# Performance work log

Measured on AMD Instinct MI355X. Metric: run time of the kernel, lower is better.

## Reference

```python
import jax, jax.numpy as jnp
import numpy as np

N_ROOMS = 300
N = N_ROOMS + 2          # state dim: 2 envelope nodes + rooms
M = N_ROOMS + 1          # input dim: [Tout; Q per room]
T = 60000                # number of t_eval points
DT = 30.0                # seconds between solution points
N_KNOTS = 2001           # Tout interpolation knots
ONE_THIRD = 1.0 / 3.0


def setup_inputs() -> dict:
    key = jax.random.key(0)
    k1, k2, k3, k4 = jax.random.split(key, 4)
    n_params = N * N + N_ROOMS
    params = jax.random.uniform(k1, (n_params,), jnp.float32)
    theta_lo = jnp.zeros((n_params,), jnp.float32)
    # conductance-like entries kept tiny so RK4 with h=30s stays stable
    theta_hi = jnp.concatenate([
        jnp.full((N * N,), 1e-4, jnp.float32),
        jnp.ones((N_ROOMS,), jnp.float32),
    ])
    B = jax.random.normal(k2, (N, M), jnp.float32) * 1e-3  # constant input matrix
    tout_t = jnp.linspace(0.0, T * DT, N_KNOTS).astype(jnp.float32)
    tout_vals = 15.0 + 10.0 * jax.random.normal(k3, (N_KNOTS,), jnp.float32)
    iv = 15.0 + 10.0 * jax.random.uniform(k4, (N, 1), jnp.float32)
    t_eval = jnp.arange(T, dtype=jnp.float32) * DT
    return {"params": params, "theta_lo": theta_lo, "theta_hi": theta_hi,
            "B": B, "tout_t": tout_t, "tout_vals": tout_vals,
            "iv": iv, "t_eval": t_eval, "t0": 0}


def reference(params, theta_lo, theta_hi, B, tout_t, tout_vals, iv, t_eval, t0):
    # transform + physical scaling of raw parameters
    x = jax.nn.sigmoid(params)
    theta = theta_lo + (theta_hi - theta_lo) * x
    W = theta[: N * N].reshape(N, N)
    # RC conductance matrix: diagonally dominant, negative diagonal (stable)
    A = W - jnp.diag(jnp.abs(W).sum(axis=1))
    Q = theta[N * N:]  # per-room heat gains [N_ROOMS]

    def f(t, y):
        # dy/dt = A y + B u,  u = [Tout(t + t0); Q]
        Tout = jnp.interp(t + t0, tout_t, tout_vals)
        u = jnp.concatenate([Tout[None], Q])[:, None]  # [M, 1]
        return A @ y + B @ u

    def step(y, th):
        # torchdiffeq method='rk4' uses the 3/8-rule (rk4_alt_step_func)
        t, h = th
        k1 = f(t, y)
        k2 = f(t + h * ONE_THIRD, y + h * ONE_THIRD * k1)
        k3 = f(t + 2.0 * h * ONE_THIRD, y + h * (k2 - ONE_THIRD * k1))
        k4 = f(t + h, y + h * (k1 - k2 + k3))
        y1 = y + (k1 + 3.0 * (k2 + k3) + k4) * (h * 0.125)
        return y1, y1

    ts = t_eval[:-1]
    hs = t_eval[1:] - t_eval[:-1]
    _, ys = jax.lax.scan(step, iv, (ts, hs))
    return jnp.concatenate([iv[None], ys], axis=0)  # [T, N, 1]
```

## Files before the change

kernel.cpp:

```cpp
#include <hip/hip_runtime.h>
#include <math.h>

#define NN     302
#define MM     301
#define NROOMS 300
#define NP     320
#define TS     59999
#define KN     2001
#define DTH    30.0f

#define L_CHUNK 256
#define N_CHUNK 235
#define N_BND   234
#define NB_PAD  240
#define N_GRP   15

#define WS_M    0
#define WS_M2   102400
#define WS_P    307200
#define WS_UV   409600
#define WS_B0C  411200
#define WS_TAU  412160
#define WS_W    652160
#define WS_G    1061760
#define WS_Y    1138560
#define WS_Z    1213760
#define WS_SA   1218880
#define WS_SB   1257280
#define WS_PL   1276480
#define WS_PA   1378880
#define WS_PB   1481280
#define WS_PT   1583680
#define WS_MT   2914880

typedef float vf2 __attribute__((ext_vector_type(2)));

#define ENGINE_BOUNDS __launch_bounds__(512) __attribute__((amdgpu_waves_per_eu(2, 2)))
#define PKFMA(acc, a, b) asm("v_pk_fma_f32 %0, %1, %2, %0" : "+v"(acc) : "v"(a), "v"(b))
#define PIN4(a, b, c, d) asm volatile("" : "+v"(a), "+v"(b), "+v"(c), "+v"(d))

__global__ __launch_bounds__(320) void buildrow_kernel(
    const float* __restrict__ params, const float* __restrict__ tlo,
    const float* __restrict__ thi, float* __restrict__ M, float* __restrict__ MT)
{
    const int r = blockIdx.x;
    const int c = threadIdx.x;
    float wv = 0.0f;
    if (r < NN && c < NN) {
        const int idx = r * NN + c;
        const float x = 1.0f / (1.0f + expf(-params[idx]));
        wv = tlo[idx] + (thi[idx] - tlo[idx]) * x;
    }
    __shared__ float red[5];
    float s = fabsf(wv);
    #pragma unroll
    for (int off = 32; off > 0; off >>= 1) s += __shfl_xor(s, off, 64);
    if ((c & 63) == 0) red[c >> 6] = s;
    __syncthreads();
    const float rs = red[0] + red[1] + red[2] + red[3] + red[4];
    float v = DTH * wv;
    if (r == c) v -= DTH * rs;
    M[r * NP + c] = v;
    MT[(size_t)c * NP + r] = v;
}

__global__ void b0c_kernel(const float* __restrict__ params,
                           const float* __restrict__ tlo,
                           const float* __restrict__ thi,
                           const float* __restrict__ B, float* __restrict__ b0c)
{
    __shared__ float Qs[NROOMS];
    const int r = blockIdx.x;
    const int l = threadIdx.x;
    for (int q = l; q < NROOMS; q += 64) {
        const int idx = NN * NN + q;
        const float x = 1.0f / (1.0f + expf(-params[idx]));
        Qs[q] = tlo[idx] + (thi[idx] - tlo[idx]) * x;
    }
    __syncthreads();
    if (r >= NN) {
        if (l == 0) { b0c[r] = 0.0f; b0c[NP + r] = 0.0f; }
        return;
    }
    float s = 0.0f;
    for (int q = l; q < NROOMS; q += 64) s = fmaf(B[r * MM + 1 + q], Qs[q], s);
    #pragma unroll
    for (int off = 32; off > 0; off >>= 1) s += __shfl_xor(s, off, 64);
    if (l == 0) { b0c[r] = B[r * MM]; b0c[NP + r] = s; }
}

__global__ void matmul4r(const float* __restrict__ A, const float* __restrict__ B,
                         float* __restrict__ C)
{
    const int c = blockIdx.x * 64 + threadIdx.x;
    const int r0 = blockIdx.y * 4;
    const float* Ar = A + (size_t)r0 * NP;
    float a0 = 0.f, a1 = 0.f, a2 = 0.f, a3 = 0.f;
    #pragma unroll 4
    for (int k = 0; k < NP; ++k) {
        const float b = B[(size_t)k * NP + c];
        a0 = fmaf(Ar[k], b, a0);
        a1 = fmaf(Ar[NP + k], b, a1);
        a2 = fmaf(Ar[2 * NP + k], b, a2);
        a3 = fmaf(Ar[3 * NP + k], b, a3);
    }
    C[(size_t)r0 * NP + c] = a0;
    C[(size_t)(r0 + 1) * NP + c] = a1;
    C[(size_t)(r0 + 2) * NP + c] = a2;
    C[(size_t)(r0 + 3) * NP + c] = a3;
}

__global__ void matmulP(const float* __restrict__ M2, const float* __restrict__ M,
                        float* __restrict__ P, float* __restrict__ PT0)
{
    const int c = blockIdx.x * 64 + threadIdx.x;
    const int r0 = blockIdx.y * 4;
    const float* Ar = M2 + (size_t)r0 * NP;
    float a0 = 0.f, a1 = 0.f, a2 = 0.f, a3 = 0.f;
    #pragma unroll 4
    for (int k = 0; k < NP; ++k) {
        const size_t o = (size_t)k * NP + c;
        const float b = (1.0f / 6.0f) * M[o] + (1.0f / 24.0f) * M2[o];
        a0 = fmaf(Ar[k], b, a0);
        a1 = fmaf(Ar[NP + k], b, a1);
        a2 = fmaf(Ar[2 * NP + k], b, a2);
        a3 = fmaf(Ar[3 * NP + k], b, a3);
    }
    float acc[4] = {a0, a1, a2, a3};
    float4 t;
    #pragma unroll
    for (int u = 0; u < 4; ++u) {
        const int r = r0 + u;
        const size_t idx = (size_t)r * NP + c;
        float v = acc[u] + M[idx] + 0.5f * M2[idx];
        if (r == c && r < NN) v += 1.0f;
        P[idx] = v;
        ((float*)&t)[u] = v;
    }
    *(float4*)(PT0 + (size_t)c * NP + r0) = t;
}

__global__ __launch_bounds__(320) void vec_kernel(
    const float* __restrict__ MT, const float* __restrict__ b0c,
    float* __restrict__ uv, const float* __restrict__ iv,
    float* __restrict__ W, float* __restrict__ out)
{
    __shared__ float ysB[NP], ysC[NP];
    const int tid = threadIdx.x;
    const float s = DTH / 8.0f;

    const float b0 = b0c[tid];
    const float cc = b0c[NP + tid];
    ysB[tid] = b0; ysC[tid] = cc;
    __syncthreads();

    float mb, mc, m2b, m2c, m3b, m3c;
    {
        float aB = 0.f, aC = 0.f;
        for (int k = 0; k < NP; ++k) {
            const float a = MT[(size_t)k * NP + tid];
            aB = fmaf(a, ysB[k], aB);
            aC = fmaf(a, ysC[k], aC);
        }
        mb = aB; mc = aC;
    }
    __syncthreads(); ysB[tid] = mb; ysC[tid] = mc; __syncthreads();
    {
        float aB = 0.f, aC = 0.f;
        for (int k = 0; k < NP; ++k) {
            const float a = MT[(size_t)k * NP + tid];
            aB = fmaf(a, ysB[k], aB);
            aC = fmaf(a, ysC[k], aC);
        }
        m2b = aB; m2c = aC;
    }
    __syncthreads(); ysB[tid] = m2b; ysC[tid] = m2c; __syncthreads();
    {
        float aB = 0.f, aC = 0.f;
        for (int k = 0; k < NP; ++k) {
            const float a = MT[(size_t)k * NP + tid];
            aB = fmaf(a, ysB[k], aB);
            aC = fmaf(a, ysC[k], aC);
        }
        m3b = aB; m3c = aC;
    }

    const float u1 = s * (b0 + mb + (1.0f / 3.0f) * (m2b + m3b));
    const float u2 = s * (3.0f * b0 + 2.0f * mb + m2b);
    const float u3 = s * (3.0f * b0 + mb);
    const float u4 = s * b0;
    const float dd = s * (8.0f * cc + 4.0f * mc + (4.0f / 3.0f) * m2c + (1.0f / 3.0f) * m3c);

    uv[tid]          = u1;
    uv[NP + tid]     = u2;
    uv[2 * NP + tid] = u3;
    uv[3 * NP + tid] = u4;
    uv[4 * NP + tid] = dd;

    W[(size_t)(0 << 8) * NP + tid] = dd;
    W[(size_t)(1 << 8) * NP + tid] = u1;
    W[(size_t)(2 << 8) * NP + tid] = u2;
    W[(size_t)(3 << 8) * NP + tid] = u3;
    W[(size_t)(4 << 8) * NP + tid] = u4;

    if (tid < NN) out[tid] = iv[tid];
}

__global__ void tau_kernel(const float* __restrict__ tout_t,
                           const float* __restrict__ tout_v,
                           const int* __restrict__ t0p,
                           float4* __restrict__ tau)
{
    const int n = blockIdx.x * 256 + threadIdx.x;
    if (n >= TS) return;
    const float tbase = 30.0f * (float)n + (float)(*t0p);
    float r[4];
    #pragma unroll
    for (int st = 0; st < 4; ++st) {
        const float x = tbase + 10.0f * (float)st;
        float res;
        if (x <= tout_t[0])            res = tout_v[0];
        else if (x >= tout_t[KN - 1])  res = tout_v[KN - 1];
        else {
            int k = (int)(x * (1.0f / 900.0f));
            if (k > KN - 2) k = KN - 2;
            if (k < 0) k = 0;
            if (x < tout_t[k] && k > 0) --k;
            else if (x >= tout_t[k + 1] && k < KN - 2) ++k;
            const float tk = tout_t[k], tk1 = tout_t[k + 1];
            const float wgt = (x - tk) / (tk1 - tk);
            res = tout_v[k] + wgt * (tout_v[k + 1] - tout_v[k]);
        }
        r[st] = res;
    }
    tau[n] = make_float4(r[0], r[1], r[2], r[3]);
}

__global__ __launch_bounds__(320) void fat_kernel(
    const float* __restrict__ src, float* __restrict__ dst,
    float* __restrict__ PTall, int j, float* __restrict__ W,
    const float* __restrict__ Sin, float* __restrict__ Sout, int npairs)
{
    const int b = blockIdx.x;
    const int tid = threadIdx.x;
    if (b < 320) {
        const int w = tid >> 6, l = tid & 63;
        const int r = (b & 63) * 5 + w;
        const int c = (b >> 6) * 64 + l;
        const float* Ar = src + (size_t)r * NP;
        float acc = 0.f;
        #pragma unroll 4
        for (int k = 0; k < NP; ++k)
            acc = fmaf(Ar[k], src[(size_t)k * NP + c], acc);
        dst[(size_t)r * NP + c] = acc;
        PTall[(size_t)(j + 1) * NP * NP + (size_t)c * NP + r] = acc;
        return;
    }
    const float* PTj = PTall + (size_t)j * NP * NP;
    const int c0 = (b - 320) * 4;
    __shared__ float ys[4][NP];
    if (j < 8) {
        const int nc = 5 << j;
        #pragma unroll
        for (int u = 0; u < 4; ++u) {
            const int ci = c0 + u;
            float val = 0.0f;
            if (ci < nc) {
                const int v = ci >> j, mo = ci & ((1 << j) - 1);
                val = W[(size_t)((v << 8) + mo) * NP + tid];
            }
            ys[u][tid] = val;
        }
        __syncthreads();
        float a0 = 0.f, a1 = 0.f, a2 = 0.f, a3 = 0.f;
        #pragma unroll 4
        for (int k = 0; k < NP; ++k) {
            const float p = PTj[(size_t)k * NP + tid];
            a0 = fmaf(p, ys[0][k], a0);
            a1 = fmaf(p, ys[1][k], a1);
            a2 = fmaf(p, ys[2][k], a2);
            a3 = fmaf(p, ys[3][k], a3);
        }
        const float acc[4] = {a0, a1, a2, a3};
        #pragma unroll
        for (int u = 0; u < 4; ++u) {
            const int ci = c0 + u;
            if (ci < nc) {
                const int v = ci >> j, mo = ci & ((1 << j) - 1);
                W[(size_t)((v << 8) + (1 << j) + mo) * NP + tid] = acc[u];
            }
        }
    } else {
        #pragma unroll
        for (int u = 0; u < 4; ++u) {
            const int k = c0 + u;
            ys[u][tid] = (k < npairs) ? Sin[(size_t)(2 * k) * NP + tid] : 0.0f;
        }
        __syncthreads();
        float a0 = 0.f, a1 = 0.f, a2 = 0.f, a3 = 0.f;
        #pragma unroll 4
        for (int k = 0; k < NP; ++k) {
            const float p = PTj[(size_t)k * NP + tid];
            a0 = fmaf(p, ys[0][k], a0);
            a1 = fmaf(p, ys[1][k], a1);
            a2 = fmaf(p, ys[2][k], a2);
            a3 = fmaf(p, ys[3][k], a3);
        }
        const float acc[4] = {a0, a1, a2, a3};
        #pragma unroll
        for (int u = 0; u < 4; ++u) {
            const int k = c0 + u;
            if (k < npairs)
                Sout[(size_t)k * NP + tid] = acc[u] + Sin[(size_t)(2 * k + 1) * NP + tid];
        }
    }
}

__global__ void gsum_kernel(const float* __restrict__ W,
                            const float4* __restrict__ tau,
                            float* __restrict__ G)
{
    const int r = blockIdx.x * 64 + threadIdx.x;
    const int c = blockIdx.y;
    if (c >= N_BND) { G[(size_t)c * NP + r] = 0.0f; return; }
    const float* W0 = W;
    const float* W1 = W + 1 * (size_t)L_CHUNK * NP;
    const float* W2 = W + 2 * (size_t)L_CHUNK * NP;
    const float* W3 = W + 3 * (size_t)L_CHUNK * NP;
    const float* W4 = W + 4 * (size_t)L_CHUNK * NP;
    const int nbase = c * L_CHUNK + L_CHUNK - 1;
    float g = 0.f;
    for (int m = 0; m < L_CHUNK; ++m) {
        const float4 a = tau[nbase - m];
        const size_t o = (size_t)m * NP + r;
        float t = W0[o];
        t = fmaf(a.x, W1[o], t);
        t = fmaf(a.y, W2[o], t);
        t = fmaf(a.z, W3[o], t);
        t = fmaf(a.w, W4[o], t);
        g += t;
    }
    G[(size_t)c * NP + r] = g;
}

__device__ __forceinline__ void load_pfrag(const float* __restrict__ Psrc,
                                           vf2 p[5][20], int l, int w)
{
    #pragma unroll
    for (int k = 0; k < 5; ++k) {
        const float* Pr = Psrc + (size_t)(l + 64 * k) * NP + 40 * w;
        #pragma unroll
        for (int j4 = 0; j4 < 10; ++j4) {
            const float4 v4 = *(const float4*)(Pr + 4 * j4);
            vf2 a; a.x = v4.x; a.y = v4.y;
            vf2 b; b.x = v4.z; b.y = v4.w;
            p[k][2 * j4] = a;
            p[k][2 * j4 + 1] = b;
        }
    }
    #pragma unroll
    for (int k = 0; k < 5; ++k)
        #pragma unroll
        for (int jj = 0; jj < 20; jj += 4)
            PIN4(p[k][jj], p[k][jj + 1], p[k][jj + 2], p[k][jj + 3]);
}

__device__ __forceinline__ void fma_phase(vf2 p[5][20], const float* __restrict__ yb,
                                          float* __restrict__ pw, int l)
{
    vf2 a0 = {0.f, 0.f}, a1 = {0.f, 0.f}, a2 = {0.f, 0.f},
        a3 = {0.f, 0.f}, a4 = {0.f, 0.f};
    #pragma unroll
    for (int j4 = 0; j4 < 10; ++j4) {
        const float4 yv = *(const float4*)(yb + 4 * j4);
        vf2 y01; y01.x = yv.x; y01.y = yv.y;
        vf2 y23; y23.x = yv.z; y23.y = yv.w;
        const int jj = 2 * j4;
        PKFMA(a0, p[0][jj], y01); PKFMA(a0, p[0][jj + 1], y23);
        PKFMA(a1, p[1][jj], y01); PKFMA(a1, p[1][jj + 1], y23);
        PKFMA(a2, p[2][jj], y01); PKFMA(a2, p[2][jj + 1], y23);
        PKFMA(a3, p[3][jj], y01); PKFMA(a3, p[3][jj + 1], y23);
        PKFMA(a4, p[4][jj], y01); PKFMA(a4, p[4][jj + 1], y23);
    }
    pw[l]       = a0.x + a0.y;
    pw[l + 64]  = a1.x + a1.y;
    pw[l + 128] = a2.x + a2.y;
    pw[l + 192] = a3.x + a3.y;
    pw[l + 256] = a4.x + a4.y;
}

__device__ __forceinline__ float reduce8(const float* __restrict__ pb, int r)
{
    float s = pb[r];
    #pragma unroll
    for (int k = 1; k < 8; ++k) s += pb[k * NP + r];
    return s;
}

__global__ ENGINE_BOUNDS void bscan_kernel(
    const float* __restrict__ PL16, const float* __restrict__ S4,
    const float* __restrict__ iv, float* __restrict__ Z)
{
    const int tid = threadIdx.x;
    const int w = tid >> 6, l = tid & 63;
    vf2 p[5][20];
    load_pfrag(PL16, p, l, w);

    __shared__ float ybuf[NP];
    __shared__ float part[2 * 8 * NP];
    __shared__ float ring[N_GRP * NP];

    const int r = 40 * w + l;
    float Sv[N_GRP];
    if (l < 40) {
        #pragma unroll
        for (int i = 0; i < N_GRP; ++i) Sv[i] = S4[(size_t)i * NP + r];
    }
    if (tid < NP) {
        const float y0 = (tid < NN) ? iv[tid] : 0.f;
        ybuf[tid] = y0;
        Z[tid] = y0;
    }
    __syncthreads();

    for (int g = 0; g < N_GRP; ++g) {
        float* pb = part + (g & 1) * 8 * NP;
        fma_phase(p, ybuf + 40 * w, pb + w * NP, l);
        __syncthreads();
        if (l < 40) {
            const float yn = reduce8(pb, r) + Sv[g];
            ybuf[r] = yn;
            ring[g * NP + r] = yn;
        }
    }
    __syncthreads();
    for (int s2 = 0; s2 < N_GRP; ++s2)
        for (int j = tid; j < NP; j += 512)
            Z[(size_t)(s2 + 1) * NP + j] = ring[s2 * NP + j];
}

__global__ ENGINE_BOUNDS void brefill_kernel(
    const float* __restrict__ PL, const float* __restrict__ G,
    const float* __restrict__ Z, float* __restrict__ Y)
{
    const int tid = threadIdx.x;
    const int w = tid >> 6, l = tid & 63;
    vf2 p[5][20];
    load_pfrag(PL, p, l, w);

    __shared__ float ybuf[NP];
    __shared__ float part[2 * 8 * NP];
    __shared__ float ring[16 * NP];

    const int g = blockIdx.x;
    const int nsteps = (16 * g + 16 <= N_BND) ? 16 : (N_BND - 16 * g);
    const int r = 40 * w + l;
    float Gv[16];
    if (l < 40) {
        for (int i = 0; i < nsteps; ++i) Gv[i] = G[(size_t)(16 * g + i) * NP + r];
    }
    if (tid < NP) {
        const float z = Z[(size_t)g * NP + tid];
        ybuf[tid] = z;
        if (g == 0) Y[tid] = z;
    }
    __syncthreads();

    for (int i = 0; i < nsteps; ++i) {
        float* pb = part + (i & 1) * 8 * NP;
        fma_phase(p, ybuf + 40 * w, pb + w * NP, l);
        __syncthreads();
        if (l < 40) {
            const float yn = reduce8(pb, r) + Gv[i];
            ybuf[r] = yn;
            ring[i * NP + r] = yn;
        }
    }
    __syncthreads();
    for (int s2 = 0; s2 < nsteps; ++s2)
        for (int j = tid; j < NP; j += 512)
            Y[(size_t)(16 * g + 1 + s2) * NP + j] = ring[s2 * NP + j];
}

__global__ ENGINE_BOUNDS void refill_kernel(
    const float* __restrict__ P, const float* __restrict__ uv,
    const float4* __restrict__ tau, const float* __restrict__ Y,
    float* __restrict__ out)
{
    const int tid = threadIdx.x;
    const int w = tid >> 6, l = tid & 63;
    vf2 p[5][20];
    load_pfrag(P, p, l, w);

    __shared__ float ybuf[NP];
    __shared__ float part[2 * 8 * NP];
    __shared__ float ring[16 * NP];
    __shared__ float4 taus[16];

    const int r = 40 * w + l;
    float du0 = 0.f, du1 = 0.f, du2 = 0.f, du3 = 0.f, dd = 0.f;
    if (l < 40) {
        du0 = uv[r]; du1 = uv[NP + r]; du2 = uv[2 * NP + r];
        du3 = uv[3 * NP + r]; dd = uv[4 * NP + r];
    }

    const int c = blockIdx.x;
    const int n0 = c * L_CHUNK;
    const int n1 = (n0 + L_CHUNK < TS) ? (n0 + L_CHUNK) : TS;
    if (tid < NP) ybuf[tid] = Y[(size_t)c * NP + tid];
    int wstart = n0;
    if (tid < 16 && n0 + tid < n1) taus[tid] = tau[n0 + tid];
    __syncthreads();

    for (int n = n0; n < n1; ++n) {
        const int slot = n - wstart;
        float* pb = part + (n & 1) * 8 * NP;
        fma_phase(p, ybuf + 40 * w, pb + w * NP, l);
        __syncthreads();
        if (l < 40) {
            const float4 a = taus[slot];
            float yn = reduce8(pb, r) + dd;
            yn = fmaf(a.x, du0, yn);
            yn = fmaf(a.y, du1, yn);
            yn = fmaf(a.z, du2, yn);
            yn = fmaf(a.w, du3, yn);
            ybuf[r] = yn;
            ring[slot * NP + r] = yn;
        }
        if (slot == 15 || n == n1 - 1) {
            __syncthreads();
            const int nrows = slot + 1;
            for (int s2 = 0; s2 < nrows; ++s2) {
                const size_t row = (size_t)(wstart + 1 + s2);
                for (int j = tid; j < NN; j += 512)
                    out[row * NN + j] = ring[s2 * NP + j];
            }
            wstart = n + 1;
            if (tid < 16 && wstart + tid < n1) taus[tid] = tau[wstart + tid];
        }
    }
}

extern "C" void kernel_launch(void* const* d_in, const int* in_sizes, int n_in,
                              void* d_out, int out_size, void* d_ws, size_t ws_size,
                              hipStream_t stream)
{
    const float* params = (const float*)d_in[0];
    const float* tlo    = (const float*)d_in[1];
    const float* thi    = (const float*)d_in[2];
    const float* B      = (const float*)d_in[3];
    const float* tout_t = (const float*)d_in[4];
    const float* tout_v = (const float*)d_in[5];
    const float* iv     = (const float*)d_in[6];
    const int*   t0     = (const int*)d_in[8];
    float* out = (float*)d_out;
    float* ws  = (float*)d_ws;

    float*  M    = ws + WS_M;
    float*  MT   = ws + WS_MT;
    float*  M2   = ws + WS_M2;
    float*  P    = ws + WS_P;
    float*  UV   = ws + WS_UV;
    float*  B0C  = ws + WS_B0C;
    float4* TAU  = (float4*)(ws + WS_TAU);
    float*  W    = ws + WS_W;
    float*  G    = ws + WS_G;
    float*  Y    = ws + WS_Y;
    float*  Z    = ws + WS_Z;
    float*  SA   = ws + WS_SA;
    float*  SB   = ws + WS_SB;
    float*  PL   = ws + WS_PL;
    float*  PA   = ws + WS_PA;
    float*  PB   = ws + WS_PB;
    float*  PT   = ws + WS_PT;

    buildrow_kernel<<<NP, NP, 0, stream>>>(params, tlo, thi, M, MT);
    b0c_kernel<<<NP, 64, 0, stream>>>(params, tlo, thi, B, B0C);

    matmul4r<<<dim3(5, 80), 64, 0, stream>>>(M, M, M2);
    matmulP<<<dim3(5, 80), 64, 0, stream>>>(M2, M, P, PT);

    vec_kernel<<<1, NP, 0, stream>>>(MT, B0C, UV, iv, W, out);
    tau_kernel<<<(TS + 255) / 256, 256, 0, stream>>>(tout_t, tout_v, t0, TAU);

    const float* Spp[5] = { G, SA, SB, SA, SB };
    const float* src = P;
    for (int j = 0; j < 8; ++j) {
        float* dst = (j == 7) ? PL : ((j & 1) ? PB : PA);
        const int aux = ((5 << j) + 3) / 4;
        fat_kernel<<<320 + aux, 320, 0, stream>>>(src, dst, PT, j, W,
                                                  nullptr, nullptr, 0);
        src = dst;
    }
    gsum_kernel<<<dim3(5, NB_PAD), 64, 0, stream>>>(W, TAU, G);
    for (int j = 8; j < 12; ++j) {
        float* dst = (j & 1) ? PB : PA;
        const int npairs = 120 >> (j - 8);
        const int aux = (npairs + 3) / 4;
        fat_kernel<<<320 + aux, 320, 0, stream>>>(src, dst, PT, j, W,
                                                  Spp[j - 8], (float*)Spp[j - 7], npairs);
        src = dst;
    }

    bscan_kernel<<<1, 512, 0, stream>>>(PB, SB, iv, Z);
    brefill_kernel<<<N_GRP, 512, 0, stream>>>(PL, G, Z, Y);

    refill_kernel<<<N_CHUNK, 512, 0, stream>>>(P, UV, TAU, Y, out);
}
```

Before: 822.9 us.

## Keep state vector in registers and broadcast via readlane instead of LDS

The per-step state y now lives in a register of the wave that owns those 40 rows, and each wave broadcasts it with readlane into SGPR operands of the packed FMAs. This removes the ybuf shared-memory write and read on the serial critical path of every step. The P fragment row mapping changes to 4*l+k so each lane writes its partial sums as one float4. Readlane sequences add scalar work and SGPR pressure, and correctness depends on the matching row permutation in the reduce layout.

```diff
diff --git a/kernel.cpp b/kernel.cpp
--- a/kernel.cpp
+++ b/kernel.cpp
@@ -36,7 +36,7 @@
 typedef float vf2 __attribute__((ext_vector_type(2)));
 
 #define ENGINE_BOUNDS __launch_bounds__(512) __attribute__((amdgpu_waves_per_eu(2, 2)))
-#define PKFMA(acc, a, b) asm("v_pk_fma_f32 %0, %1, %2, %0" : "+v"(acc) : "v"(a), "v"(b))
+#define PKFMA_S(acc, a, s) asm("v_pk_fma_f32 %0, %1, %2, %0" : "+v"(acc) : "v"(a), "s"(s))
 #define PIN4(a, b, c, d) asm volatile("" : "+v"(a), "+v"(b), "+v"(c), "+v"(d))
 
 __global__ __launch_bounds__(320) void buildrow_kernel(
@@ -348,7 +348,8 @@
 {
     #pragma unroll
     for (int k = 0; k < 5; ++k) {
-        const float* Pr = Psrc + (size_t)(l + 64 * k) * NP + 40 * w;
+        const int row = (k < 4) ? (4 * l + k) : (256 + l);
+        const float* Pr = Psrc + (size_t)row * NP + 40 * w;
         #pragma unroll
         for (int j4 = 0; j4 < 10; ++j4) {
             const float4 v4 = *(const float4*)(Pr + 4 * j4);
@@ -365,28 +366,33 @@
             PIN4(p[k][jj], p[k][jj + 1], p[k][jj + 2], p[k][jj + 3]);
 }
 
-__device__ __forceinline__ void fma_phase(vf2 p[5][20], const float* __restrict__ yb,
+__device__ __forceinline__ void fma_phase(const vf2 p[5][20], float yn,
                                           float* __restrict__ pw, int l)
 {
     vf2 a0 = {0.f, 0.f}, a1 = {0.f, 0.f}, a2 = {0.f, 0.f},
         a3 = {0.f, 0.f}, a4 = {0.f, 0.f};
+    const int yi = __float_as_int(yn);
     #pragma unroll
     for (int j4 = 0; j4 < 10; ++j4) {
-        const float4 yv = *(const float4*)(yb + 4 * j4);
-        vf2 y01; y01.x = yv.x; y01.y = yv.y;
-        vf2 y23; y23.x = yv.z; y23.y = yv.w;
+        vf2 y01, y23;
+        y01.x = __int_as_float(__builtin_amdgcn_readlane(yi, 4 * j4 + 0));
+        y01.y = __int_as_float(__builtin_amdgcn_readlane(yi, 4 * j4 + 1));
+        y23.x = __int_as_float(__builtin_amdgcn_readlane(yi, 4 * j4 + 2));
+        y23.y = __int_as_float(__builtin_amdgcn_readlane(yi, 4 * j4 + 3));
         const int jj = 2 * j4;
-        PKFMA(a0, p[0][jj], y01); PKFMA(a0, p[0][jj + 1], y23);
-        PKFMA(a1, p[1][jj], y01); PKFMA(a1, p[1][jj + 1], y23);
-        PKFMA(a2, p[2][jj], y01); PKFMA(a2, p[2][jj + 1], y23);
-        PKFMA(a3, p[3][jj], y01); PKFMA(a3, p[3][jj + 1], y23);
-        PKFMA(a4, p[4][jj], y01); PKFMA(a4, p[4][jj + 1], y23);
-    }
-    pw[l]       = a0.x + a0.y;
-    pw[l + 64]  = a1.x + a1.y;
-    pw[l + 128] = a2.x + a2.y;
-    pw[l + 192] = a3.x + a3.y;
-    pw[l + 256] = a4.x + a4.y;
+        PKFMA_S(a0, p[0][jj], y01); PKFMA_S(a0, p[0][jj + 1], y23);
+        PKFMA_S(a1, p[1][jj], y01); PKFMA_S(a1, p[1][jj + 1], y23);
+        PKFMA_S(a2, p[2][jj], y01); PKFMA_S(a2, p[2][jj + 1], y23);
+        PKFMA_S(a3, p[3][jj], y01); PKFMA_S(a3, p[3][jj + 1], y23);
+        PKFMA_S(a4, p[4][jj], y01); PKFMA_S(a4, p[4][jj + 1], y23);
+    }
+    float4 h4;
+    h4.x = a0.x + a0.y;
+    h4.y = a1.x + a1.y;
+    h4.z = a2.x + a2.y;
+    h4.w = a3.x + a3.y;
+    *(float4*)(pw + 4 * l) = h4;
+    pw[256 + l] = a4.x + a4.y;
 }
 
 __device__ __forceinline__ float reduce8(const float* __restrict__ pb, int r)
@@ -406,32 +412,30 @@
     vf2 p[5][20];
     load_pfrag(PL16, p, l, w);
 
-    __shared__ float ybuf[NP];
     __shared__ float part[2 * 8 * NP];
     __shared__ float ring[N_GRP * NP];
 
     const int r = 40 * w + l;
+    const int rr = 40 * w + (l < 40 ? l : 39);
     float Sv[N_GRP];
+    #pragma unroll
+    for (int i = 0; i < N_GRP; ++i) Sv[i] = 0.f;
     if (l < 40) {
         #pragma unroll
         for (int i = 0; i < N_GRP; ++i) Sv[i] = S4[(size_t)i * NP + r];
     }
-    if (tid < NP) {
-        const float y0 = (tid < NN) ? iv[tid] : 0.f;
-        ybuf[tid] = y0;
-        Z[tid] = y0;
-    }
-    __syncthreads();
+    float yn = 0.f;
+    if (l < 40) {
+        yn = (r < NN) ? iv[r] : 0.f;
+        Z[r] = yn;
+    }
 
     for (int g = 0; g < N_GRP; ++g) {
         float* pb = part + (g & 1) * 8 * NP;
-        fma_phase(p, ybuf + 40 * w, pb + w * NP, l);
+        fma_phase(p, yn, pb + w * NP, l);
         __syncthreads();
-        if (l < 40) {
-            const float yn = reduce8(pb, r) + Sv[g];
-            ybuf[r] = yn;
-            ring[g * NP + r] = yn;
-        }
+        yn = reduce8(pb, rr) + Sv[g];
+        if (l < 40) ring[g * NP + r] = yn;
     }
     __syncthreads();
     for (int s2 = 0; s2 < N_GRP; ++s2)
@@ -448,33 +452,31 @@
     vf2 p[5][20];
     load_pfrag(PL, p, l, w);
 
-    __shared__ float ybuf[NP];
     __shared__ float part[2 * 8 * NP];
     __shared__ float ring[16 * NP];
 
     const int g = blockIdx.x;
     const int nsteps = (16 * g + 16 <= N_BND) ? 16 : (N_BND - 16 * g);
     const int r = 40 * w + l;
+    const int rr = 40 * w + (l < 40 ? l : 39);
     float Gv[16];
+    #pragma unroll
+    for (int i = 0; i < 16; ++i) Gv[i] = 0.f;
     if (l < 40) {
         for (int i = 0; i < nsteps; ++i) Gv[i] = G[(size_t)(16 * g + i) * NP + r];
     }
-    if (tid < NP) {
-        const float z = Z[(size_t)g * NP + tid];
-        ybuf[tid] = z;
-        if (g == 0) Y[tid] = z;
-    }
-    __syncthreads();
+    float yn = 0.f;
+    if (l < 40) {
+        yn = Z[(size_t)g * NP + r];
+        if (g == 0) Y[r] = yn;
+    }
 
     for (int i = 0; i < nsteps; ++i) {
         float* pb = part + (i & 1) * 8 * NP;
-        fma_phase(p, ybuf + 40 * w, pb + w * NP, l);
+        fma_phase(p, yn, pb + w * NP, l);
         __syncthreads();
-        if (l < 40) {
-            const float yn = reduce8(pb, r) + Gv[i];
-            ybuf[r] = yn;
-            ring[i * NP + r] = yn;
-        }
+        yn = reduce8(pb, rr) + Gv[i];
+        if (l < 40) ring[i * NP + r] = yn;
     }
     __syncthreads();
     for (int s2 = 0; s2 < nsteps; ++s2)
@@ -492,12 +494,12 @@
     vf2 p[5][20];
     load_pfrag(P, p, l, w);
 
-    __shared__ float ybuf[NP];
     __shared__ float part[2 * 8 * NP];
     __shared__ float ring[16 * NP];
     __shared__ float4 taus[16];
 
     const int r = 40 * w + l;
+    const int rr = 40 * w + (l < 40 ? l : 39);
     float du0 = 0.f, du1 = 0.f, du2 = 0.f, du3 = 0.f, dd = 0.f;
     if (l < 40) {
         du0 = uv[r]; du1 = uv[NP + r]; du2 = uv[2 * NP + r];
@@ -507,7 +509,7 @@
     const int c = blockIdx.x;
     const int n0 = c * L_CHUNK;
     const int n1 = (n0 + L_CHUNK < TS) ? (n0 + L_CHUNK) : TS;
-    if (tid < NP) ybuf[tid] = Y[(size_t)c * NP + tid];
+    float yn = (l < 40) ? Y[(size_t)c * NP + r] : 0.f;
     int wstart = n0;
     if (tid < 16 && n0 + tid < n1) taus[tid] = tau[n0 + tid];
     __syncthreads();
@@ -515,18 +517,16 @@
     for (int n = n0; n < n1; ++n) {
         const int slot = n - wstart;
         float* pb = part + (n & 1) * 8 * NP;
-        fma_phase(p, ybuf + 40 * w, pb + w * NP, l);
+        fma_phase(p, yn, pb + w * NP, l);
         __syncthreads();
-        if (l < 40) {
-            const float4 a = taus[slot];
-            float yn = reduce8(pb, r) + dd;
-            yn = fmaf(a.x, du0, yn);
-            yn = fmaf(a.y, du1, yn);
-            yn = fmaf(a.z, du2, yn);
-            yn = fmaf(a.w, du3, yn);
-            ybuf[r] = yn;
-            ring[slot * NP + r] = yn;
-        }
+        const float4 a = taus[slot];
+        float t = reduce8(pb, rr) + dd;
+        t = fmaf(a.x, du0, t);
+        t = fmaf(a.y, du1, t);
+        t = fmaf(a.z, du2, t);
+        t = fmaf(a.w, du3, t);
+        yn = t;
+        if (l < 40) ring[slot * NP + r] = yn;
         if (slot == 15 || n == n1 - 1) {
             __syncthreads();
             const int nrows = slot + 1;
```

Measured after the change: 843.8 us. 2.5% more time.
